# Kernel optimization log

Measured on AMD Instinct MI355X. Metric: run time of the kernel, lower is better.

Reference implementation:

```python
import jax, jax.numpy as jnp
import numpy as np

HIDDEN = 1024
N_HEAD = 16
HEAD_DIM = HIDDEN // N_HEAD
ROPE_THETA = 10000.0


def setup_inputs() -> dict:
    key = jax.random.key(0)
    ks = jax.random.split(key, 6)
    B, T = 4, 2048
    x = jax.random.normal(ks[0], (B, T, HIDDEN), dtype=jnp.float32)
    rnn_state = jax.random.normal(ks[1], (B, HIDDEN), dtype=jnp.float32)
    Wqkv = jax.random.normal(ks[2], (HIDDEN, 3 * HIDDEN), dtype=jnp.float32) * 0.02
    bqkv = jnp.zeros((3 * HIDDEN,), dtype=jnp.float32)
    Wproj = jax.random.normal(ks[3], (HIDDEN, HIDDEN), dtype=jnp.float32) * 0.02
    bproj = jnp.zeros((HIDDEN,), dtype=jnp.float32)
    return {"x": x, "rnn_state": rnn_state, "Wqkv": Wqkv, "bqkv": bqkv,
            "Wproj": Wproj, "bproj": bproj}


def _rope_tables(T, dtype):
    # GPT-NeoX style half-split RoPE
    inv_freq = 1.0 / (ROPE_THETA ** (jnp.arange(0, HEAD_DIM, 2, dtype=jnp.float32) / HEAD_DIM))
    freqs = jnp.arange(T, dtype=jnp.float32)[:, None] * inv_freq[None, :]  # [T, D/2]
    return jnp.cos(freqs).astype(dtype), jnp.sin(freqs).astype(dtype)


def _apply_rope(x, cos, sin):
    # x: [B, H, T, D]; cos/sin: [T, D/2]
    x1, x2 = jnp.split(x, 2, axis=-1)
    c = cos[None, None, :, :]
    s = sin[None, None, :, :]
    return jnp.concatenate([x1 * c - x2 * s, x1 * s + x2 * c], axis=-1)


def reference(x, rnn_state, Wqkv, bqkv, Wproj, bproj):
    B, T, C = x.shape
    qkv = x @ Wqkv + bqkv  # [B, T, 3C]
    q, k, v = jnp.split(qkv, 3, axis=-1)
    # split heads -> [B, H, T, D]
    def heads(t):
        return t.reshape(B, T, N_HEAD, HEAD_DIM).transpose(0, 2, 1, 3)
    q, k, v = heads(q), heads(k), heads(v)
    cos, sin = _rope_tables(T, x.dtype)
    q = _apply_rope(q, cos, sin)
    k = _apply_rope(k, cos, sin)
    scale = 1.0 / jnp.sqrt(jnp.asarray(HEAD_DIM, dtype=x.dtype))
    scores = jnp.einsum('bhtd,bhsd->bhts', q, k) * scale  # [B,H,T,T]
    # causal additive mask: 0 on/below diag, -inf above (matches torch buffer)
    causal = jnp.tril(jnp.ones((T, T), dtype=bool))
    scores = jnp.where(causal[None, None, :, :], scores, -jnp.inf)
    attn = jax.nn.softmax(scores, axis=-1)
    out = jnp.einsum('bhts,bhsd->bhtd', attn, v)  # [B,H,T,D]
    out = out.transpose(0, 2, 1, 3).reshape(B, T, C)
    output = out @ Wproj + bproj
    return (output, rnn_state)
```

## Files before the change

kernel.cpp:

```cpp
#include <hip/hip_runtime.h>
#include <cstdint>
#include <cstddef>
#include <math.h>

typedef unsigned short u16;
typedef __attribute__((ext_vector_type(8))) short short8;
typedef __attribute__((ext_vector_type(4))) float floatx4;

#define HIDDEN 1024
#define NHEAD 16
#define HD 64
#define BB 4
#define TT 2048
#define MM (BB*TT)
#define NQKV 3072
#define NEGINF (-30000.0f)

__device__ inline u16 f2bf(float f){
  union { float f; unsigned u; } v; v.f = f;
  unsigned r = v.u + 0x7FFFu + ((v.u >> 16) & 1u);
  return (u16)(r >> 16);
}
__device__ inline void load_lds16(const void* g, void* l){
  __builtin_amdgcn_global_load_lds((const __attribute__((address_space(1))) void*)g,
                                   (__attribute__((address_space(3))) void*)l,
                                   16, 0, 0);
}
__device__ inline short8 cvt8(const float* p){
  const floatx4 a = *(const floatx4*)p;
  const floatx4 b = *(const floatx4*)(p + 4);
  union { short8 s; unsigned u[4]; } r;
  asm("v_cvt_pk_bf16_f32 %0, %1, %2" : "=v"(r.u[0]) : "v"(a[0]), "v"(a[1]));
  asm("v_cvt_pk_bf16_f32 %0, %1, %2" : "=v"(r.u[1]) : "v"(a[2]), "v"(a[3]));
  asm("v_cvt_pk_bf16_f32 %0, %1, %2" : "=v"(r.u[2]) : "v"(b[0]), "v"(b[1]));
  asm("v_cvt_pk_bf16_f32 %0, %1, %2" : "=v"(r.u[3]) : "v"(b[2]), "v"(b[3]));
  return r.s;
}

__global__ void rope_tables(float* __restrict__ cosT, float* __restrict__ sinT){
  const int idx = blockIdx.x * 256 + threadIdx.x;
  const int t = idx >> 5, f = idx & 31;
  const float inv = powf(10000.0f, -(float)f * (1.0f / 32.0f));
  const float ang = (float)t * inv;
  cosT[idx] = cosf(ang);
  sinT[idx] = sinf(ang);
}

__global__ void convert_x(const float* __restrict__ in, u16* __restrict__ outp){
  const int i = (blockIdx.x * 256 + threadIdx.x) * 8;
  #pragma unroll
  for (int u = 0; u < 8; u++) outp[i + u] = f2bf(in[i + u]);
}

__global__ void transpose_f32_bf16(const float* __restrict__ in, u16* __restrict__ out,
                                   int R, int C){
  __shared__ alignas(16) u16 tile[32][33];
  const int c0 = blockIdx.x * 32, r0 = blockIdx.y * 32;
  const int tx = threadIdx.x & 31, ty = threadIdx.x >> 5;
  for (int i = ty; i < 32; i += 8)
    tile[i][tx] = f2bf(in[(size_t)(r0 + i) * C + c0 + tx]);
  __syncthreads();
  for (int i = ty; i < 32; i += 8) out[(size_t)(c0 + i) * R + r0 + tx] = tile[tx][i];
}

__global__ void gemm_qkv(const u16* __restrict__ X, const u16* __restrict__ WT,
                         const float* __restrict__ bias,
                         const float* __restrict__ ropeC, const float* __restrict__ ropeS,
                         u16* __restrict__ Qb, u16* __restrict__ Kb, u16* __restrict__ Vtg)
{
  __shared__ alignas(16) u16 As[128 * 32];
  __shared__ alignas(16) u16 Bs[128 * 32];
  __shared__ alignas(16) u16 VTx[4][64 * 24];
  const int tid = threadIdx.x;
  const int wid = tid >> 6, lane = tid & 63;
  const int quad = lane >> 4, ln = lane & 15;
  const int row0 = blockIdx.y * 128, col0 = blockIdx.x * 128;
  const int wm = (wid >> 1) * 64, wn = (wid & 1) * 64;
  floatx4 acc[4][4] = {};

  const int sr = tid >> 2, sk = (tid & 3) * 8;

  for (int kk = 0; kk < 32; ++kk){
    const int k0 = kk * 32;
    __syncthreads();
    load_lds16(&X [(size_t)(row0 + sr      ) * 1024 + k0 + sk], &As[(size_t)(tid      ) * 8]);
    load_lds16(&X [(size_t)(row0 + sr + 64 ) * 1024 + k0 + sk], &As[(size_t)(tid + 256) * 8]);
    load_lds16(&WT[(size_t)(col0 + sr      ) * 1024 + k0 + sk], &Bs[(size_t)(tid      ) * 8]);
    load_lds16(&WT[(size_t)(col0 + sr + 64 ) * 1024 + k0 + sk], &Bs[(size_t)(tid + 256) * 8]);
    __syncthreads();
    short8 a[4], b[4];
    #pragma unroll
    for (int i = 0; i < 4; i++) a[i] = *(const short8*)&As[(wm + i*16 + ln) * 32 + quad * 8];
    #pragma unroll
    for (int j = 0; j < 4; j++) b[j] = *(const short8*)&Bs[(wn + j*16 + ln) * 32 + quad * 8];
    #pragma unroll
    for (int i = 0; i < 4; i++)
      #pragma unroll
      for (int j = 0; j < 4; j++)
        acc[i][j] = __builtin_amdgcn_mfma_f32_16x16x32_bf16(a[i], b[j], acc[i][j], 0, 0, 0);
  }

  const int wcol0 = col0 + wn;
  const int which = wcol0 >> 10;
  const int h = (wcol0 & 1023) >> 6;
  float bs[4];
  #pragma unroll
  for (int j = 0; j < 4; j++) bs[j] = bias[wcol0 + j*16 + ln];

  if (which < 2){
    #pragma unroll
    for (int i = 0; i < 4; i++){
      #pragma unroll
      for (int rr = 0; rr < 4; rr++){
        const int rowg = row0 + wm + i*16 + quad*4 + rr;
        const int b_ = rowg >> 11, t = rowg & 2047;
        u16* op = (which == 0 ? Qb : Kb) + ((size_t)(b_ * NHEAD + h) * TT + t) * HD;
        #pragma unroll
        for (int j = 0; j < 2; j++){
          const int f = j*16 + ln;
          const float cs = ropeC[t * 32 + f];
          const float sn = ropeS[t * 32 + f];
          const float x1 = acc[i][j  ][rr] + bs[j  ];
          const float x2 = acc[i][j+2][rr] + bs[j+2];
          float y1 = x1 * cs - x2 * sn;
          float y2 = x1 * sn + x2 * cs;
          if (which == 0){ y1 *= 0.125f; y2 *= 0.125f; }
          op[f]      = f2bf(y1);
          op[f + 32] = f2bf(y2);
        }
      }
    }
  } else {
    #pragma unroll
    for (int i = 0; i < 4; i++){
      #pragma unroll
      for (int j = 0; j < 4; j++)
        #pragma unroll
        for (int rr = 0; rr < 4; rr++)
          VTx[wid][(j*16 + ln) * 24 + quad*4 + rr] = f2bf(acc[i][j][rr] + bs[j]);
      asm volatile("s_waitcnt lgkmcnt(0)" ::: "memory");
      const int d = lane;
      const short8 v0 = *(const short8*)&VTx[wid][d * 24 + 0];
      const short8 v1 = *(const short8*)&VTx[wid][d * 24 + 8];
      const int rowg = row0 + wm + i*16;
      const int b_ = rowg >> 11, t0 = rowg & 2047;
      u16* vp = &Vtg[((size_t)(b_ * NHEAD + h) * HD + d) * TT + t0];
      *(short8*)&vp[0] = v0;
      *(short8*)&vp[8] = v1;
      asm volatile("s_waitcnt lgkmcnt(0)" ::: "memory");
    }
  }
}

__global__ void __launch_bounds__(256, 4)
attn(const u16* __restrict__ Qb, const u16* __restrict__ Kb,
     const u16* __restrict__ Vtg, u16* __restrict__ AO)
{
  const int bh = blockIdx.x, tbi = 15 - (int)blockIdx.y;
  const int tid = threadIdx.x;
  const int wid = tid >> 6, lane = tid & 63;
  const int quad = lane >> 4, ln = lane & 15;

  __shared__ alignas(16) u16 Kl[64 * 72];
  __shared__ alignas(16) u16 Vt[64 * 72];
  __shared__ alignas(16) float Plf[4][16 * 72];

  const u16* Qh = Qb  + (size_t)bh * TT * HD;
  const u16* Kh = Kb  + (size_t)bh * TT * HD;
  const u16* Vh = Vtg + (size_t)bh * HD * TT;
  const int b_ = bh >> 4, h = bh & 15;

  const int qbase = tbi * 128 + wid * 32;

  short8 aq[2][2];
  #pragma unroll
  for (int qt = 0; qt < 2; qt++){
    aq[qt][0] = *(const short8*)&Qh[(size_t)(qbase + qt*16 + ln) * HD + quad*8];
    aq[qt][1] = *(const short8*)&Qh[(size_t)(qbase + qt*16 + ln) * HD + 32 + quad*8];
  }

  floatx4 o[2][4] = {};
  float l_i[2][4] = {};
  float* Pf = &Plf[wid][0];

  const int nch = 2 * (tbi + 1);
  for (int ch = 0; ch < nch; ++ch){
    const int key0 = ch * 64;
    __syncthreads();
    #pragma unroll
    for (int it = 0; it < 2; ++it){
      const int idx = it * 256 + tid;
      const int r = idx >> 3, c8 = (idx & 7) * 8;
      *(short8*)&Kl[r * 72 + c8] = *(const short8*)&Kh[(size_t)(key0 + r) * HD + c8];
      *(short8*)&Vt[r * 72 + c8] = *(const short8*)&Vh[(size_t)r * TT + key0 + c8];
    }
    __syncthreads();

    if (key0 <= qbase + 31){
      const bool act0 = (key0 <= qbase + 15);
      short8 pk0[2], pk1[2];
      #pragma unroll
      for (int qt = 0; qt < 2; qt++){
        if (qt == 0 && !act0) continue;
        const int qt0 = qbase + qt*16;
        floatx4 z[4];
        #pragma unroll
        for (int j = 0; j < 4; j++){
          const short8 kb0 = *(const short8*)&Kl[(j*16 + ln) * 72 + quad*8];
          const short8 kb1 = *(const short8*)&Kl[(j*16 + ln) * 72 + 32 + quad*8];
          floatx4 zz = {0.0f, 0.0f, 0.0f, 0.0f};
          zz = __builtin_amdgcn_mfma_f32_16x16x32_bf16(aq[qt][0], kb0, zz, 0, 0, 0);
          zz = __builtin_amdgcn_mfma_f32_16x16x32_bf16(aq[qt][1], kb1, zz, 0, 0, 0);
          z[j] = zz;
        }
        if (key0 + 63 > qt0){
          #pragma unroll
          for (int j = 0; j < 4; j++)
            #pragma unroll
            for (int rr = 0; rr < 4; rr++){
              const int key = key0 + j*16 + ln;
              const int t   = qt0 + quad*4 + rr;
              if (key > t) z[j][rr] = NEGINF;
            }
        }
        #pragma unroll
        for (int j = 0; j < 4; j++)
          #pragma unroll
          for (int rr = 0; rr < 4; rr++){
            const float p = __expf(z[j][rr]);
            l_i[qt][rr] += p;
            Pf[(quad*4 + rr) * 72 + j*16 + ln] = p;
          }
        asm volatile("s_waitcnt lgkmcnt(0)" ::: "memory");
        pk0[qt] = cvt8(&Pf[ln * 72 + quad*8]);
        pk1[qt] = cvt8(&Pf[ln * 72 + 32 + quad*8]);
      }
      #pragma unroll
      for (int n = 0; n < 4; n++){
        const short8 vb0 = *(const short8*)&Vt[(n*16 + ln) * 72 + quad*8];
        const short8 vb1 = *(const short8*)&Vt[(n*16 + ln) * 72 + 32 + quad*8];
        if (act0){
          o[0][n] = __builtin_amdgcn_mfma_f32_16x16x32_bf16(pk0[0], vb0, o[0][n], 0, 0, 0);
          o[0][n] = __builtin_amdgcn_mfma_f32_16x16x32_bf16(pk1[0], vb1, o[0][n], 0, 0, 0);
        }
        o[1][n] = __builtin_amdgcn_mfma_f32_16x16x32_bf16(pk0[1], vb0, o[1][n], 0, 0, 0);
        o[1][n] = __builtin_amdgcn_mfma_f32_16x16x32_bf16(pk1[1], vb1, o[1][n], 0, 0, 0);
      }
    }
  }

  #pragma unroll
  for (int qt = 0; qt < 2; qt++)
    #pragma unroll
    for (int rr = 0; rr < 4; rr++){
      float rs = l_i[qt][rr];
      #pragma unroll
      for (int off = 1; off < 16; off <<= 1) rs += __shfl_xor(rs, off);
      l_i[qt][rr] = rs;
    }

  #pragma unroll
  for (int qt = 0; qt < 2; qt++)
    #pragma unroll
    for (int n = 0; n < 4; n++)
      #pragma unroll
      for (int rr = 0; rr < 4; rr++){
        const int t = qbase + qt*16 + quad*4 + rr;
        const float inv_l = 1.0f / fmaxf(l_i[qt][rr], 1e-20f);
        AO[(size_t)(b_ * TT + t) * HIDDEN + h * HD + n*16 + ln] = f2bf(o[qt][n][rr] * inv_l);
      }
}

__global__ void gemm_proj(const u16* __restrict__ A, const u16* __restrict__ WT,
                          const float* __restrict__ bias, float* __restrict__ out)
{
  __shared__ alignas(16) u16 As[128 * 32];
  __shared__ alignas(16) u16 Bs[128 * 32];
  const int tid = threadIdx.x;
  const int wid = tid >> 6, lane = tid & 63;
  const int quad = lane >> 4, ln = lane & 15;
  const int row0 = blockIdx.y * 128, col0 = blockIdx.x * 128;
  const int wm = (wid >> 1) * 64, wn = (wid & 1) * 64;
  floatx4 acc[4][4] = {};

  const int sr = tid >> 2, sk = (tid & 3) * 8;

  for (int kk = 0; kk < 32; ++kk){
    const int k0 = kk * 32;
    __syncthreads();
    load_lds16(&A [(size_t)(row0 + sr      ) * 1024 + k0 + sk], &As[(size_t)(tid      ) * 8]);
    load_lds16(&A [(size_t)(row0 + sr + 64 ) * 1024 + k0 + sk], &As[(size_t)(tid + 256) * 8]);
    load_lds16(&WT[(size_t)(col0 + sr      ) * 1024 + k0 + sk], &Bs[(size_t)(tid      ) * 8]);
    load_lds16(&WT[(size_t)(col0 + sr + 64 ) * 1024 + k0 + sk], &Bs[(size_t)(tid + 256) * 8]);
    __syncthreads();
    short8 a[4], b[4];
    #pragma unroll
    for (int i = 0; i < 4; i++) a[i] = *(const short8*)&As[(wm + i*16 + ln) * 32 + quad * 8];
    #pragma unroll
    for (int j = 0; j < 4; j++) b[j] = *(const short8*)&Bs[(wn + j*16 + ln) * 32 + quad * 8];
    #pragma unroll
    for (int i = 0; i < 4; i++)
      #pragma unroll
      for (int j = 0; j < 4; j++)
        acc[i][j] = __builtin_amdgcn_mfma_f32_16x16x32_bf16(a[i], b[j], acc[i][j], 0, 0, 0);
  }

  float bs[4];
  #pragma unroll
  for (int j = 0; j < 4; j++) bs[j] = bias[col0 + wn + j*16 + ln];
  #pragma unroll
  for (int i = 0; i < 4; i++)
    #pragma unroll
    for (int rr = 0; rr < 4; rr++){
      const int rowg = row0 + wm + i*16 + quad*4 + rr;
      #pragma unroll
      for (int j = 0; j < 4; j++)
        out[(size_t)rowg * HIDDEN + col0 + wn + j*16 + ln] = acc[i][j][rr] + bs[j];
    }
}

__global__ void copy_tail(const float* __restrict__ rnn, float* __restrict__ out){
  const int i = blockIdx.x * 256 + threadIdx.x;
  if (i < BB * HIDDEN) out[(size_t)MM * HIDDEN + i] = rnn[i];
}

extern "C" void kernel_launch(void* const* d_in, const int* in_sizes, int n_in,
                              void* d_out, int out_size, void* d_ws, size_t ws_size,
                              hipStream_t stream)
{
  const float* x     = (const float*)d_in[0];
  const float* rnn   = (const float*)d_in[1];
  const float* Wqkv  = (const float*)d_in[2];
  const float* bqkv  = (const float*)d_in[3];
  const float* Wproj = (const float*)d_in[4];
  const float* bproj = (const float*)d_in[5];
  float* out = (float*)d_out;

  char* ws = (char*)d_ws;
  size_t off = 0;
  float* ropeC  = (float*)(ws + off); off += (size_t)TT * 32 * 4;
  float* ropeS  = (float*)(ws + off); off += (size_t)TT * 32 * 4;
  u16*   xN     = (u16*)(ws + off);   off += (size_t)MM * HIDDEN * 2;
  u16*   WqkvT  = (u16*)(ws + off);   off += (size_t)NQKV * HIDDEN * 2;
  u16*   WprojT = (u16*)(ws + off);   off += (size_t)HIDDEN * HIDDEN * 2;
  u16*   Qb     = (u16*)(ws + off);   off += (size_t)MM * HIDDEN * 2;
  u16*   Kb     = (u16*)(ws + off);   off += (size_t)MM * HIDDEN * 2;
  u16*   Vtg    = (u16*)(ws + off);   off += (size_t)MM * HIDDEN * 2;
  u16*   AO     = (u16*)(ws + off);   off += (size_t)MM * HIDDEN * 2;

  rope_tables<<<(TT * 32) / 256, 256, 0, stream>>>(ropeC, ropeS);
  convert_x<<<(MM * HIDDEN) / (256 * 8), 256, 0, stream>>>(x, xN);
  transpose_f32_bf16<<<dim3(NQKV / 32, HIDDEN / 32), 256, 0, stream>>>(Wqkv, WqkvT, HIDDEN, NQKV);
  transpose_f32_bf16<<<dim3(HIDDEN / 32, HIDDEN / 32), 256, 0, stream>>>(Wproj, WprojT, HIDDEN, HIDDEN);
  gemm_qkv<<<dim3(NQKV / 128, MM / 128), 256, 0, stream>>>(xN, WqkvT, bqkv, ropeC, ropeS, Qb, Kb, Vtg);
  attn<<<dim3(BB * NHEAD, 16), 256, 0, stream>>>(Qb, Kb, Vtg, AO);
  gemm_proj<<<dim3(HIDDEN / 128, MM / 128), 256, 0, stream>>>(AO, WprojT, bproj, out);
  copy_tail<<<(BB * HIDDEN + 255) / 256, 256, 0, stream>>>(rnn, out);
}
```

Before: 274.3 us.

## Double-buffer K/V tiles in attention with register prefetch

```diff
diff --git a/kernel.cpp b/kernel.cpp
--- a/kernel.cpp
+++ b/kernel.cpp
@@ -152,7 +152,7 @@
   }
 }
 
-__global__ void __launch_bounds__(256, 4)
+__global__ void __launch_bounds__(256, 3)
 attn(const u16* __restrict__ Qb, const u16* __restrict__ Kb,
      const u16* __restrict__ Vtg, u16* __restrict__ AO)
 {
@@ -161,9 +161,9 @@
   const int wid = tid >> 6, lane = tid & 63;
   const int quad = lane >> 4, ln = lane & 15;
 
-  __shared__ alignas(16) u16 Kl[64 * 72];
-  __shared__ alignas(16) u16 Vt[64 * 72];
-  __shared__ alignas(16) float Plf[4][16 * 72];
+  __shared__ alignas(16) u16 Kl2[2][64 * 72];
+  __shared__ alignas(16) u16 Vt2[2][64 * 72];
+  __shared__ alignas(16) float Plf[4][16 * 68];
 
   const u16* Qh = Qb  + (size_t)bh * TT * HD;
   const u16* Kh = Kb  + (size_t)bh * TT * HD;
@@ -183,20 +183,35 @@
   float l_i[2][4] = {};
   float* Pf = &Plf[wid][0];
 
+  const int pr = tid >> 3, pc = (tid & 7) * 8;
+  short8 kpre0, kpre1, vpre0, vpre1;
+
   const int nch = 2 * (tbi + 1);
+
+  kpre0 = *(const short8*)&Kh[(size_t)(pr     ) * HD + pc];
+  kpre1 = *(const short8*)&Kh[(size_t)(pr + 32) * HD + pc];
+  vpre0 = *(const short8*)&Vh[(size_t)(pr     ) * TT + pc];
+  vpre1 = *(const short8*)&Vh[(size_t)(pr + 32) * TT + pc];
+  *(short8*)&Kl2[0][(pr     ) * 72 + pc] = kpre0;
+  *(short8*)&Kl2[0][(pr + 32) * 72 + pc] = kpre1;
+  *(short8*)&Vt2[0][(pr     ) * 72 + pc] = vpre0;
+  *(short8*)&Vt2[0][(pr + 32) * 72 + pc] = vpre1;
+  __syncthreads();
+
+  int cur = 0;
   for (int ch = 0; ch < nch; ++ch){
     const int key0 = ch * 64;
-    __syncthreads();
-    #pragma unroll
-    for (int it = 0; it < 2; ++it){
-      const int idx = it * 256 + tid;
-      const int r = idx >> 3, c8 = (idx & 7) * 8;
-      *(short8*)&Kl[r * 72 + c8] = *(const short8*)&Kh[(size_t)(key0 + r) * HD + c8];
-      *(short8*)&Vt[r * 72 + c8] = *(const short8*)&Vh[(size_t)r * TT + key0 + c8];
-    }
-    __syncthreads();
+    if (ch + 1 < nch){
+      const int nk0 = key0 + 64;
+      kpre0 = *(const short8*)&Kh[(size_t)(nk0 + pr     ) * HD + pc];
+      kpre1 = *(const short8*)&Kh[(size_t)(nk0 + pr + 32) * HD + pc];
+      vpre0 = *(const short8*)&Vh[(size_t)(pr     ) * TT + nk0 + pc];
+      vpre1 = *(const short8*)&Vh[(size_t)(pr + 32) * TT + nk0 + pc];
+    }
 
     if (key0 <= qbase + 31){
+      const u16* Kl = Kl2[cur];
+      const u16* Vt = Vt2[cur];
       const bool act0 = (key0 <= qbase + 15);
       short8 pk0[2], pk1[2];
       #pragma unroll
@@ -229,11 +244,11 @@
           for (int rr = 0; rr < 4; rr++){
             const float p = __expf(z[j][rr]);
             l_i[qt][rr] += p;
-            Pf[(quad*4 + rr) * 72 + j*16 + ln] = p;
+            Pf[(quad*4 + rr) * 68 + j*16 + ln] = p;
           }
         asm volatile("s_waitcnt lgkmcnt(0)" ::: "memory");
-        pk0[qt] = cvt8(&Pf[ln * 72 + quad*8]);
-        pk1[qt] = cvt8(&Pf[ln * 72 + 32 + quad*8]);
+        pk0[qt] = cvt8(&Pf[ln * 68 + quad*8]);
+        pk1[qt] = cvt8(&Pf[ln * 68 + 32 + quad*8]);
       }
       #pragma unroll
       for (int n = 0; n < 4; n++){
@@ -247,6 +262,15 @@
         o[1][n] = __builtin_amdgcn_mfma_f32_16x16x32_bf16(pk1[1], vb1, o[1][n], 0, 0, 0);
       }
     }
+
+    if (ch + 1 < nch){
+      *(short8*)&Kl2[cur ^ 1][(pr     ) * 72 + pc] = kpre0;
+      *(short8*)&Kl2[cur ^ 1][(pr + 32) * 72 + pc] = kpre1;
+      *(short8*)&Vt2[cur ^ 1][(pr     ) * 72 + pc] = vpre0;
+      *(short8*)&Vt2[cur ^ 1][(pr + 32) * 72 + pc] = vpre1;
+    }
+    __syncthreads();
+    cur ^= 1;
   }
 
   #pragma unroll
```

Measured after the change: 274.1 us. Within noise of the previous version (-0.1%).
